# Performance work log

Measured on AMD Instinct MI355X. Metric: run time of the kernel, lower is better.

The kernel has to match this reference:

```python
import jax, jax.numpy as jnp
import numpy as np

NUM_LATENTS = 32768
NUM_EMBEDDINGS = 1024
EMBEDDING_SIZE = 64


def setup_inputs() -> dict:
    key = jax.random.key(0)
    kx, ke = jax.random.split(key)
    x = jax.random.normal(kx, (NUM_LATENTS * EMBEDDING_SIZE,), dtype=jnp.float32)
    # uniform init in [-limit, limit], limit = sqrt(3/embedding_size) as in the torch module
    limit = float(np.sqrt(3.0 / EMBEDDING_SIZE))
    embeddings = jax.random.uniform(
        ke, (NUM_EMBEDDINGS, EMBEDDING_SIZE), dtype=jnp.float32,
        minval=-limit, maxval=limit)
    return {"x": x, "embeddings": embeddings}


def reference(x, embeddings):
    K, E = embeddings.shape
    x_ = x.reshape(-1, E)  # [L, E]
    # squared distances ||x - e||^2 expanded: faithful to sum((x-e)**2, -1), fused as one GEMM
    d = (
        jnp.sum(x_ * x_, axis=-1, keepdims=True)
        - 2.0 * jnp.einsum('le,ke->lk', x_, embeddings)
        + jnp.sum(embeddings * embeddings, axis=-1)
    )  # [L, K]
    indices = jnp.argmin(d, axis=-1)          # [L]
    quantized = embeddings[indices].reshape(-1)  # [L*E]
    # straight-through estimator: x + (q - stop_grad(x))
    z_hat = x + quantized - jax.lax.stop_gradient(x)
    # outputs mirror the torch dict: z_continuous, z_quantized, z_hat, z_indices
    return x, quantized, z_hat, indices
```

## Files before the change

kernel.cpp:

```cpp
#include <hip/hip_runtime.h>

#define L_TOTAL   32768
#define E_DIM     64
#define K_TOTAL   1024
#define NT_TOTAL  64
#define OUT_STRIDE 2097152
#define XPAD      68

#define NT_WORDS  1280

typedef _Float16 half_t;
typedef _Float16 half8  __attribute__((ext_vector_type(8)));
typedef float    floatx4 __attribute__((ext_vector_type(4)));

__global__ __launch_bounds__(128)
void vq_swizzle_kernel(const float* __restrict__ emb, float* __restrict__ ebuf) {
    __shared__ float s_p[128];
    __shared__ float s_n[16];
    const int nt   = blockIdx.x;
    const int t    = threadIdx.x;
    const int kt   = t >> 6;
    const int lane = t & 63;
    const int q    = lane >> 4;
    const int ln   = lane & 15;

    const float* src = emb + (size_t)(nt * 16 + ln) * E_DIM + kt * 32 + q * 8;
    float4 v0 = *(const float4*)src;
    float4 v1 = *(const float4*)(src + 4);
    float f[8] = {v0.x, v0.y, v0.z, v0.w, v1.x, v1.y, v1.z, v1.w};

    half8 h, l;
    float s = 0.f;
    #pragma unroll
    for (int j = 0; j < 8; ++j) {
        half_t hh = (half_t)f[j];
        half_t ll = (half_t)(f[j] - (float)hh);
        h[j] = hh;
        l[j] = ll;
        s = fmaf(f[j], f[j], s);
    }
    float* rec = ebuf + (size_t)nt * NT_WORDS;
    *(half8*)(rec + kt * 256 + lane * 4)       = h;
    *(half8*)(rec + 512 + kt * 256 + lane * 4) = l;

    s_p[t] = s;
    __syncthreads();
    if (t < 16) {
        float n = 0.f;
        #pragma unroll
        for (int u = 0; u < 8; ++u)
            n += s_p[(u >> 2) * 64 + (u & 3) * 16 + t];
        s_n[t] = n;
    }
    __syncthreads();
    if (t < 64) rec[1024 + t] = s_n[t & 15];
}

__global__ __launch_bounds__(256, 4)
void vq_fused_kernel(const float* __restrict__ x,
                     const float* __restrict__ emb,
                     const float* __restrict__ ebuf,
                     float* __restrict__ out) {
    __shared__ float s_x[32 * XPAD];
    __shared__ float s_best[4][32];
    __shared__ int   s_bidx[4][32];
    __shared__ int   s_fin[32];

    const int tid   = threadIdx.x;
    const int ks    = tid >> 6;
    const int lane  = tid & 63;
    const int q     = lane >> 4;
    const int ln    = lane & 15;
    const int mbase = blockIdx.x * 32;
    const int rot   = blockIdx.x & 15;
    const int nt0   = ks * 16;

    {
        const float4* xg = (const float4*)(x + (size_t)mbase * E_DIM);
        #pragma unroll
        for (int i = 0; i < 2; ++i) {
            const int f   = i * 256 + tid;
            const int row = f >> 4;
            const int col = (f & 15) * 4;
            *(float4*)(&s_x[row * XPAD + col]) = xg[f];
        }
    }
    __syncthreads();

    half8 A[2][2][2];
    floatx4 xq[2];
    #pragma unroll
    for (int rt = 0; rt < 2; ++rt) {
        const float* xr = &s_x[(rt * 16 + ln) * XPAD + q * 8];
        float sn = 0.f;
        #pragma unroll
        for (int kt = 0; kt < 2; ++kt) {
            float4 v0 = *(const float4*)(xr + kt * 32);
            float4 v1 = *(const float4*)(xr + kt * 32 + 4);
            float f[8] = {v0.x, v0.y, v0.z, v0.w, v1.x, v1.y, v1.z, v1.w};
            #pragma unroll
            for (int j = 0; j < 8; ++j) {
                half_t hh = (half_t)f[j];
                half_t ll = (half_t)(f[j] - (float)hh);
                A[rt][kt][0][j] = hh;
                A[rt][kt][1][j] = ll;
                sn = fmaf(f[j], f[j], sn);
            }
        }
        sn += __shfl_xor(sn, 16, 64);
        sn += __shfl_xor(sn, 32, 64);
        #pragma unroll
        for (int r = 0; r < 4; ++r)
            xq[rt][r] = __shfl(sn, q * 4 + r, 64);
    }

    float best[2][4];
    int   bidx[2][4];
    #pragma unroll
    for (int rt = 0; rt < 2; ++rt)
        #pragma unroll
        for (int r = 0; r < 4; ++r) { best[rt][r] = 3.402823466e+38f; bidx[rt][r] = 0x7fffffff; }

    half8 a0, a1, a2, a3; float ae;
    half8 b0, b1, b2, b3; float be;
    int nt_a, nt_b;
    {
        nt_a = nt0 + rot;
        nt_a = nt0 + (rot & 15);
        nt_a = nt0 + ((0 + rot) & 15);
        const float* rec = ebuf + (size_t)nt_a * NT_WORDS;
        a0 = *(const half8*)(rec + lane * 4);
        a1 = *(const half8*)(rec + 256 + lane * 4);
        a2 = *(const half8*)(rec + 512 + lane * 4);
        a3 = *(const half8*)(rec + 768 + lane * 4);
        ae = rec[1024 + lane];
    }

    #pragma unroll 1
    for (int j = 0; j < 16; j += 2) {
        nt_b = nt0 + ((j + 1 + rot) & 15);
        {
            const float* rec = ebuf + (size_t)nt_b * NT_WORDS;
            b0 = *(const half8*)(rec + lane * 4);
            b1 = *(const half8*)(rec + 256 + lane * 4);
            b2 = *(const half8*)(rec + 512 + lane * 4);
            b3 = *(const half8*)(rec + 768 + lane * 4);
            be = rec[1024 + lane];
        }
        {
            const int kg = nt_a * 16 + ln;
            #pragma unroll
            for (int rt = 0; rt < 2; ++rt) {
                floatx4 Ca = {0.f, 0.f, 0.f, 0.f};
                floatx4 Cb = {0.f, 0.f, 0.f, 0.f};
                Ca = __builtin_amdgcn_mfma_f32_16x16x32_f16(A[rt][0][0], a0, Ca, 0, 0, 0);
                Ca = __builtin_amdgcn_mfma_f32_16x16x32_f16(A[rt][1][0], a1, Ca, 0, 0, 0);
                Cb = __builtin_amdgcn_mfma_f32_16x16x32_f16(A[rt][0][1], a0, Cb, 0, 0, 0);
                Cb = __builtin_amdgcn_mfma_f32_16x16x32_f16(A[rt][1][1], a1, Cb, 0, 0, 0);
                Cb = __builtin_amdgcn_mfma_f32_16x16x32_f16(A[rt][0][0], a2, Cb, 0, 0, 0);
                Cb = __builtin_amdgcn_mfma_f32_16x16x32_f16(A[rt][1][0], a3, Cb, 0, 0, 0);
                #pragma unroll
                for (int r = 0; r < 4; ++r) {
                    float dot = Ca[r] + Cb[r];
                    float d = __fadd_rn(__fsub_rn(xq[rt][r], __fmul_rn(2.0f, dot)), ae);
                    if (d < best[rt][r] || (d == best[rt][r] && kg < bidx[rt][r])) {
                        best[rt][r] = d; bidx[rt][r] = kg;
                    }
                }
            }
        }
        if (j + 2 < 16) {
            nt_a = nt0 + ((j + 2 + rot) & 15);
            const float* rec = ebuf + (size_t)nt_a * NT_WORDS;
            a0 = *(const half8*)(rec + lane * 4);
            a1 = *(const half8*)(rec + 256 + lane * 4);
            a2 = *(const half8*)(rec + 512 + lane * 4);
            a3 = *(const half8*)(rec + 768 + lane * 4);
            ae = rec[1024 + lane];
        }
        {
            const int kg = nt_b * 16 + ln;
            #pragma unroll
            for (int rt = 0; rt < 2; ++rt) {
                floatx4 Ca = {0.f, 0.f, 0.f, 0.f};
                floatx4 Cb = {0.f, 0.f, 0.f, 0.f};
                Ca = __builtin_amdgcn_mfma_f32_16x16x32_f16(A[rt][0][0], b0, Ca, 0, 0, 0);
                Ca = __builtin_amdgcn_mfma_f32_16x16x32_f16(A[rt][1][0], b1, Ca, 0, 0, 0);
                Cb = __builtin_amdgcn_mfma_f32_16x16x32_f16(A[rt][0][1], b0, Cb, 0, 0, 0);
                Cb = __builtin_amdgcn_mfma_f32_16x16x32_f16(A[rt][1][1], b1, Cb, 0, 0, 0);
                Cb = __builtin_amdgcn_mfma_f32_16x16x32_f16(A[rt][0][0], b2, Cb, 0, 0, 0);
                Cb = __builtin_amdgcn_mfma_f32_16x16x32_f16(A[rt][1][0], b3, Cb, 0, 0, 0);
                #pragma unroll
                for (int r = 0; r < 4; ++r) {
                    float dot = Ca[r] + Cb[r];
                    float d = __fadd_rn(__fsub_rn(xq[rt][r], __fmul_rn(2.0f, dot)), be);
                    if (d < best[rt][r] || (d == best[rt][r] && kg < bidx[rt][r])) {
                        best[rt][r] = d; bidx[rt][r] = kg;
                    }
                }
            }
        }
    }

    #pragma unroll
    for (int o = 1; o < 16; o <<= 1) {
        #pragma unroll
        for (int rt = 0; rt < 2; ++rt)
            #pragma unroll
            for (int r = 0; r < 4; ++r) {
                float ob = __shfl_xor(best[rt][r], o, 64);
                int   oi = __shfl_xor(bidx[rt][r], o, 64);
                if (ob < best[rt][r] || (ob == best[rt][r] && oi < bidx[rt][r])) {
                    best[rt][r] = ob; bidx[rt][r] = oi;
                }
            }
    }
    if (ln == 0) {
        #pragma unroll
        for (int rt = 0; rt < 2; ++rt)
            #pragma unroll
            for (int r = 0; r < 4; ++r) {
                s_best[ks][rt * 16 + q * 4 + r] = best[rt][r];
                s_bidx[ks][rt * 16 + q * 4 + r] = bidx[rt][r];
            }
    }
    __syncthreads();

    if (tid < 32) {
        float b = 3.402823466e+38f;
        int   i = 0x7fffffff;
        #pragma unroll
        for (int s = 0; s < 4; ++s) {
            float pb = s_best[s][tid];
            int   pi = s_bidx[s][tid];
            if (pb < b || (pb == b && pi < i)) { b = pb; i = pi; }
        }
        s_fin[tid] = i;
        out[3 * (size_t)OUT_STRIDE + mbase + tid] = (float)i;
    }
    __syncthreads();

    {
        const size_t fb = (size_t)mbase * (E_DIM / 4);
        float4* o0 = (float4*)out + fb;
        float4* o1 = (float4*)(out + OUT_STRIDE) + fb;
        float4* o2 = (float4*)(out + 2 * (size_t)OUT_STRIDE) + fb;
        #pragma unroll
        for (int i = 0; i < 2; ++i) {
            const int f   = i * 256 + tid;
            const int row = f >> 4;
            const int col = (f & 15) * 4;
            const float4 xv = *(const float4*)(&s_x[row * XPAD + col]);
            const int idx = s_fin[row];
            const float4 qv = *(const float4*)(emb + (size_t)idx * E_DIM + col);
            float4 z;
            z.x = __fsub_rn(__fadd_rn(xv.x, qv.x), xv.x);
            z.y = __fsub_rn(__fadd_rn(xv.y, qv.y), xv.y);
            z.z = __fsub_rn(__fadd_rn(xv.z, qv.z), xv.z);
            z.w = __fsub_rn(__fadd_rn(xv.w, qv.w), xv.w);
            o0[f] = xv;
            o1[f] = qv;
            o2[f] = z;
        }
    }
}

extern "C" void kernel_launch(void* const* d_in, const int* in_sizes, int n_in,
                              void* d_out, int out_size, void* d_ws, size_t ws_size,
                              hipStream_t stream) {
    const float* x   = (const float*)d_in[0];
    const float* emb = (const float*)d_in[1];
    float* out  = (float*)d_out;
    float* ebuf = (float*)d_ws;

    hipLaunchKernelGGL(vq_swizzle_kernel, dim3(NT_TOTAL), dim3(128), 0, stream,
                       emb, ebuf);
    hipLaunchKernelGGL(vq_fused_kernel, dim3(L_TOTAL / 32), dim3(256), 0, stream,
                       x, emb, ebuf, out);
}
```

Baseline: 87.93 us.

## Replicate swizzled codebook and triple-buffer fully unrolled codebook loads

The preprocessing kernel now writes eight copies of the swizzled fp16 hi/lo codebook, and each fused block reads the copy selected by its block index. The aim is to spread cache and channel traffic from many blocks hitting the same addresses. The main loop is fully unrolled with three register buffers to prefetch two tiles ahead, and all 16 norm values are loaded up front. Occupancy is lowered to 3 blocks per CU to fit the extra registers, which adds eight times the ebuf footprint and write traffic and assumes ebuf was allocated large enough.

```diff
diff --git a/kernel.cpp b/kernel.cpp
--- a/kernel.cpp
+++ b/kernel.cpp
@@ -8,6 +8,8 @@
 #define XPAD      68
 
 #define NT_WORDS  1280
+#define REP       8
+#define REP_WORDS (NT_TOTAL * NT_WORDS)
 
 typedef _Float16 half_t;
 typedef _Float16 half8  __attribute__((ext_vector_type(8)));
@@ -39,11 +41,15 @@
         l[j] = ll;
         s = fmaf(f[j], f[j], s);
     }
-    float* rec = ebuf + (size_t)nt * NT_WORDS;
-    *(half8*)(rec + kt * 256 + lane * 4)       = h;
-    *(half8*)(rec + 512 + kt * 256 + lane * 4) = l;
-
     s_p[t] = s;
+
+    #pragma unroll
+    for (int c = 0; c < REP; ++c) {
+        float* rec = ebuf + (size_t)c * REP_WORDS + (size_t)nt * NT_WORDS;
+        *(half8*)(rec + kt * 256 + lane * 4)       = h;
+        *(half8*)(rec + 512 + kt * 256 + lane * 4) = l;
+    }
+
     __syncthreads();
     if (t < 16) {
         float n = 0.f;
@@ -53,10 +59,14 @@
         s_n[t] = n;
     }
     __syncthreads();
-    if (t < 64) rec[1024 + t] = s_n[t & 15];
+    if (t < 64) {
+        #pragma unroll
+        for (int c = 0; c < REP; ++c)
+            ebuf[(size_t)c * REP_WORDS + (size_t)nt * NT_WORDS + 1024 + t] = s_n[t & 15];
+    }
 }
 
-__global__ __launch_bounds__(256, 4)
+__global__ __launch_bounds__(256, 3)
 void vq_fused_kernel(const float* __restrict__ x,
                      const float* __restrict__ emb,
                      const float* __restrict__ ebuf,
@@ -74,6 +84,24 @@
     const int mbase = blockIdx.x * 32;
     const int rot   = blockIdx.x & 15;
     const int nt0   = ks * 16;
+    const float* eb = ebuf + (size_t)(blockIdx.x & (REP - 1)) * REP_WORDS;
+
+#define NTI(J) (nt0 + (((J) + rot) & 15))
+#define LOADB(B0, B1, B2, B3, J) {                                            \
+        const float* rec_ = eb + (size_t)NTI(J) * NT_WORDS;                   \
+        B0 = *(const half8*)(rec_ + lane * 4);                                \
+        B1 = *(const half8*)(rec_ + 256 + lane * 4);                          \
+        B2 = *(const half8*)(rec_ + 512 + lane * 4);                          \
+        B3 = *(const half8*)(rec_ + 768 + lane * 4); }
+
+    half8 a0, a1, a2, a3, b0, b1, b2, b3, c0, c1, c2, c3;
+    LOADB(a0, a1, a2, a3, 0)
+    LOADB(b0, b1, b2, b3, 1)
+    LOADB(c0, c1, c2, c3, 2)
+    float nv[16];
+    #pragma unroll
+    for (int j = 0; j < 16; ++j)
+        nv[j] = eb[(size_t)NTI(j) * NT_WORDS + 1024 + lane];
 
     {
         const float4* xg = (const float4*)(x + (size_t)mbase * E_DIM);
@@ -121,86 +149,50 @@
         #pragma unroll
         for (int r = 0; r < 4; ++r) { best[rt][r] = 3.402823466e+38f; bidx[rt][r] = 0x7fffffff; }
 
-    half8 a0, a1, a2, a3; float ae;
-    half8 b0, b1, b2, b3; float be;
-    int nt_a, nt_b;
-    {
-        nt_a = nt0 + rot;
-        nt_a = nt0 + (rot & 15);
-        nt_a = nt0 + ((0 + rot) & 15);
-        const float* rec = ebuf + (size_t)nt_a * NT_WORDS;
-        a0 = *(const half8*)(rec + lane * 4);
-        a1 = *(const half8*)(rec + 256 + lane * 4);
-        a2 = *(const half8*)(rec + 512 + lane * 4);
-        a3 = *(const half8*)(rec + 768 + lane * 4);
-        ae = rec[1024 + lane];
-    }
-
-    #pragma unroll 1
-    for (int j = 0; j < 16; j += 2) {
-        nt_b = nt0 + ((j + 1 + rot) & 15);
-        {
-            const float* rec = ebuf + (size_t)nt_b * NT_WORDS;
-            b0 = *(const half8*)(rec + lane * 4);
-            b1 = *(const half8*)(rec + 256 + lane * 4);
-            b2 = *(const half8*)(rec + 512 + lane * 4);
-            b3 = *(const half8*)(rec + 768 + lane * 4);
-            be = rec[1024 + lane];
-        }
-        {
-            const int kg = nt_a * 16 + ln;
-            #pragma unroll
-            for (int rt = 0; rt < 2; ++rt) {
-                floatx4 Ca = {0.f, 0.f, 0.f, 0.f};
-                floatx4 Cb = {0.f, 0.f, 0.f, 0.f};
-                Ca = __builtin_amdgcn_mfma_f32_16x16x32_f16(A[rt][0][0], a0, Ca, 0, 0, 0);
-                Ca = __builtin_amdgcn_mfma_f32_16x16x32_f16(A[rt][1][0], a1, Ca, 0, 0, 0);
-                Cb = __builtin_amdgcn_mfma_f32_16x16x32_f16(A[rt][0][1], a0, Cb, 0, 0, 0);
-                Cb = __builtin_amdgcn_mfma_f32_16x16x32_f16(A[rt][1][1], a1, Cb, 0, 0, 0);
-                Cb = __builtin_amdgcn_mfma_f32_16x16x32_f16(A[rt][0][0], a2, Cb, 0, 0, 0);
-                Cb = __builtin_amdgcn_mfma_f32_16x16x32_f16(A[rt][1][0], a3, Cb, 0, 0, 0);
-                #pragma unroll
-                for (int r = 0; r < 4; ++r) {
-                    float dot = Ca[r] + Cb[r];
-                    float d = __fadd_rn(__fsub_rn(xq[rt][r], __fmul_rn(2.0f, dot)), ae);
-                    if (d < best[rt][r] || (d == best[rt][r] && kg < bidx[rt][r])) {
-                        best[rt][r] = d; bidx[rt][r] = kg;
-                    }
-                }
-            }
-        }
-        if (j + 2 < 16) {
-            nt_a = nt0 + ((j + 2 + rot) & 15);
-            const float* rec = ebuf + (size_t)nt_a * NT_WORDS;
-            a0 = *(const half8*)(rec + lane * 4);
-            a1 = *(const half8*)(rec + 256 + lane * 4);
-            a2 = *(const half8*)(rec + 512 + lane * 4);
-            a3 = *(const half8*)(rec + 768 + lane * 4);
-            ae = rec[1024 + lane];
-        }
-        {
-            const int kg = nt_b * 16 + ln;
-            #pragma unroll
-            for (int rt = 0; rt < 2; ++rt) {
-                floatx4 Ca = {0.f, 0.f, 0.f, 0.f};
-                floatx4 Cb = {0.f, 0.f, 0.f, 0.f};
-                Ca = __builtin_amdgcn_mfma_f32_16x16x32_f16(A[rt][0][0], b0, Ca, 0, 0, 0);
-                Ca = __builtin_amdgcn_mfma_f32_16x16x32_f16(A[rt][1][0], b1, Ca, 0, 0, 0);
-                Cb = __builtin_amdgcn_mfma_f32_16x16x32_f16(A[rt][0][1], b0, Cb, 0, 0, 0);
-                Cb = __builtin_amdgcn_mfma_f32_16x16x32_f16(A[rt][1][1], b1, Cb, 0, 0, 0);
-                Cb = __builtin_amdgcn_mfma_f32_16x16x32_f16(A[rt][0][0], b2, Cb, 0, 0, 0);
-                Cb = __builtin_amdgcn_mfma_f32_16x16x32_f16(A[rt][1][0], b3, Cb, 0, 0, 0);
-                #pragma unroll
-                for (int r = 0; r < 4; ++r) {
-                    float dot = Ca[r] + Cb[r];
-                    float d = __fadd_rn(__fsub_rn(xq[rt][r], __fmul_rn(2.0f, dot)), be);
-                    if (d < best[rt][r] || (d == best[rt][r] && kg < bidx[rt][r])) {
-                        best[rt][r] = d; bidx[rt][r] = kg;
-                    }
-                }
-            }
-        }
-    }
+#define STEP(B0, B1, B2, B3, J) {                                             \
+        const int nt_ = NTI(J);                                               \
+        const int kg_ = nt_ * 16 + ln;                                        \
+        const float env_ = nv[J];                                             \
+        _Pragma("unroll")                                                     \
+        for (int rt = 0; rt < 2; ++rt) {                                      \
+            floatx4 Ca = {0.f, 0.f, 0.f, 0.f};                                \
+            floatx4 Cb = {0.f, 0.f, 0.f, 0.f};                                \
+            Ca = __builtin_amdgcn_mfma_f32_16x16x32_f16(A[rt][0][0], B0, Ca, 0, 0, 0); \
+            Ca = __builtin_amdgcn_mfma_f32_16x16x32_f16(A[rt][1][0], B1, Ca, 0, 0, 0); \
+            Cb = __builtin_amdgcn_mfma_f32_16x16x32_f16(A[rt][0][1], B0, Cb, 0, 0, 0); \
+            Cb = __builtin_amdgcn_mfma_f32_16x16x32_f16(A[rt][1][1], B1, Cb, 0, 0, 0); \
+            Cb = __builtin_amdgcn_mfma_f32_16x16x32_f16(A[rt][0][0], B2, Cb, 0, 0, 0); \
+            Cb = __builtin_amdgcn_mfma_f32_16x16x32_f16(A[rt][1][0], B3, Cb, 0, 0, 0); \
+            _Pragma("unroll")                                                 \
+            for (int r = 0; r < 4; ++r) {                                     \
+                float dot = Ca[r] + Cb[r];                                    \
+                float d = __fadd_rn(__fsub_rn(xq[rt][r], __fmul_rn(2.0f, dot)), env_); \
+                if (d < best[rt][r] || (d == best[rt][r] && kg_ < bidx[rt][r])) {      \
+                    best[rt][r] = d; bidx[rt][r] = kg_;                       \
+                }                                                             \
+            }                                                                 \
+        } }
+
+    STEP(a0, a1, a2, a3, 0)  LOADB(a0, a1, a2, a3, 3)
+    STEP(b0, b1, b2, b3, 1)  LOADB(b0, b1, b2, b3, 4)
+    STEP(c0, c1, c2, c3, 2)  LOADB(c0, c1, c2, c3, 5)
+    STEP(a0, a1, a2, a3, 3)  LOADB(a0, a1, a2, a3, 6)
+    STEP(b0, b1, b2, b3, 4)  LOADB(b0, b1, b2, b3, 7)
+    STEP(c0, c1, c2, c3, 5)  LOADB(c0, c1, c2, c3, 8)
+    STEP(a0, a1, a2, a3, 6)  LOADB(a0, a1, a2, a3, 9)
+    STEP(b0, b1, b2, b3, 7)  LOADB(b0, b1, b2, b3, 10)
+    STEP(c0, c1, c2, c3, 8)  LOADB(c0, c1, c2, c3, 11)
+    STEP(a0, a1, a2, a3, 9)  LOADB(a0, a1, a2, a3, 12)
+    STEP(b0, b1, b2, b3, 10) LOADB(b0, b1, b2, b3, 13)
+    STEP(c0, c1, c2, c3, 11) LOADB(c0, c1, c2, c3, 14)
+    STEP(a0, a1, a2, a3, 12) LOADB(a0, a1, a2, a3, 15)
+    STEP(b0, b1, b2, b3, 13)
+    STEP(c0, c1, c2, c3, 14)
+    STEP(a0, a1, a2, a3, 15)
+
+#undef STEP
+#undef LOADB
+#undef NTI
 
     #pragma unroll
     for (int o = 1; o < 16; o <<= 1) {
```

Result: slower. 93.45 us (+6.3%).
